# Performance work log

Hardware: AMD Instinct MI355X
Metric: run time of the kernel (lower is better)

## Reference

```python
import jax, jax.numpy as jnp
import numpy as np

D_IN = 16
D_OUT = 8
HIDDEN = 64


def setup_inputs() -> dict:
    key = jax.random.key(0)
    ks = jax.random.split(key, 8)
    B = 524288
    x = jax.random.normal(ks[0], (B, D_IN), dtype=jnp.float32)
    # scalar attention weights for the two attention blocks, shape [2, 1]
    wq = jax.random.normal(ks[1], (2, 1), dtype=jnp.float32)
    wk = jax.random.normal(ks[2], (2, 1), dtype=jnp.float32)
    wv = jax.random.normal(ks[3], (2, 1), dtype=jnp.float32)
    # hidden: Linear(16 -> HIDDEN), output: Linear(HIDDEN -> 8)
    lim_h = 1.0 / np.sqrt(D_IN)
    Wh = jax.random.uniform(ks[4], (HIDDEN, D_IN), minval=-lim_h, maxval=lim_h, dtype=jnp.float32)
    bh = jax.random.uniform(ks[5], (HIDDEN,), minval=-lim_h, maxval=lim_h, dtype=jnp.float32)
    lim_o = 1.0 / np.sqrt(HIDDEN)
    Wo = jax.random.uniform(ks[6], (D_OUT, HIDDEN), minval=-lim_o, maxval=lim_o, dtype=jnp.float32)
    bo = jax.random.uniform(ks[7], (D_OUT,), minval=-lim_o, maxval=lim_o, dtype=jnp.float32)
    return {"x": x, "wq": wq, "wk": wk, "wv": wv, "Wh": Wh, "bh": bh, "Wo": Wo, "bo": bo}


def _self_attention(x, q, k, v):
    # x: [B, D]; q, k, v: scalars. Q=K=V are scalar-scaled copies of x.
    Q = q * x  # [B, D]
    K = k * x
    V = v * x
    # Alpha[b, i, j] = K[b, i] * Q[b, j]  (outer product, matches Kt @ Q)
    Alpha = K[:, :, None] * Q[:, None, :]  # [B, D, D]
    A = jax.nn.softmax(Alpha, axis=2)
    # O[b, j] = sum_i V[b, i] * A[b, i, j]  (matches V @ AlphaD)
    return jnp.einsum('bi,bij->bj', V, A)  # [B, D]


def reference(x, wq, wk, wv, Wh, bh, Wo, bo):
    o1 = _self_attention(x[:, 0:16], wq[0, 0], wk[0, 0], wv[0, 0])  # [B, 16]
    x1 = jax.nn.sigmoid(o1 @ Wh.T + bh)                              # [B, HIDDEN]
    x2 = x1 @ Wo.T + bo                                              # [B, 8]
    o2 = _self_attention(x2, wq[1, 0], wk[1, 0], wv[1, 0])          # [B, 8]
    w = jax.nn.softmax(o2, axis=1)                                   # [B, 8]
    # out = x[:, None, 8:16] @ w[:, :, None]  -> [B, 1, 1]
    out = jnp.einsum('bi,bi->b', x[:, 8:16], w)[:, None, None]
    return out
```

## Files before the change

kernel.cpp:

```cpp
#include <hip/hip_runtime.h>


typedef float v2f __attribute__((ext_vector_type(2)));

#define LOG2E 1.44269504088896340736f
#define ROWS 4

__device__ __forceinline__ float rcpf(float a) { return __builtin_amdgcn_rcpf(a); }

#if __has_builtin(__builtin_amdgcn_exp2f)
__device__ __forceinline__ float exp2_fast(float a) { return __builtin_amdgcn_exp2f(a); }
#else
__device__ __forceinline__ float exp2_fast(float a) { return __expf(0.6931471805599453f * a); }
#endif

__global__ __launch_bounds__(256, 2) void fused_attn_mlp(
    const float* __restrict__ x,
    const float* __restrict__ wq,
    const float* __restrict__ wk,
    const float* __restrict__ wv,
    const float* __restrict__ Wh,
    const float* __restrict__ bh,
    const float* __restrict__ Wo,
    const float* __restrict__ bo,
    float* __restrict__ out,
    int B)
{
    const int t = threadIdx.x;
    const int b0 = blockIdx.x * (256 * ROWS) + t;

    bool valid[ROWS];
    #pragma unroll
    for (int r = 0; r < ROWS; ++r) valid[r] = (b0 + r * 256) < B;

    float4 xraw[ROWS][4];
    #pragma unroll
    for (int r = 0; r < ROWS; ++r) {
        if (valid[r]) {
            const float4* xr = reinterpret_cast<const float4*>(x) + (size_t)(b0 + r * 256) * 4;
            xraw[r][0] = xr[0]; xraw[r][1] = xr[1]; xraw[r][2] = xr[2]; xraw[r][3] = xr[3];
        } else {
            xraw[r][0] = xraw[r][1] = xraw[r][2] = xraw[r][3] = float4{0.f,0.f,0.f,0.f};
        }
    }

    __shared__ float sWh[64 * 16];
    __shared__ float sWoT[64 * 8];
    __shared__ float sbh[64];
    {
        const float4* src = reinterpret_cast<const float4*>(Wh);
        float4* dst = reinterpret_cast<float4*>(sWh);
        dst[t] = src[t];
    }
    #pragma unroll
    for (int r = t; r < 512; r += 256) {
        const int h = r >> 3, o = r & 7;
        sWoT[h * 8 + o] = Wo[o * 64 + h];
    }
    if (t < 64) sbh[t] = bh[t];
    __syncthreads();

    float xs[ROWS][16];
    v2f xv2[ROWS][8];
    #pragma unroll
    for (int r = 0; r < ROWS; ++r) {
        xs[r][0]=xraw[r][0].x; xs[r][1]=xraw[r][0].y; xs[r][2]=xraw[r][0].z; xs[r][3]=xraw[r][0].w;
        xs[r][4]=xraw[r][1].x; xs[r][5]=xraw[r][1].y; xs[r][6]=xraw[r][1].z; xs[r][7]=xraw[r][1].w;
        xs[r][8]=xraw[r][2].x; xs[r][9]=xraw[r][2].y; xs[r][10]=xraw[r][2].z; xs[r][11]=xraw[r][2].w;
        xs[r][12]=xraw[r][3].x; xs[r][13]=xraw[r][3].y; xs[r][14]=xraw[r][3].z; xs[r][15]=xraw[r][3].w;
        #pragma unroll
        for (int p = 0; p < 8; ++p) { v2f v; v[0]=xs[r][2*p]; v[1]=xs[r][2*p+1]; xv2[r][p]=v; }
    }

    const float kq1 = wk[0] * wq[0] * LOG2E;
    const float v1  = wv[0];

    float xmx[ROWS], xmn[ROWS];
    #pragma unroll
    for (int r = 0; r < ROWS; ++r) {
        float mx = xs[r][0], mn = xs[r][0];
        #pragma unroll
        for (int i = 1; i < 16; ++i) { mx = fmaxf(mx, xs[r][i]); mn = fminf(mn, xs[r][i]); }
        xmx[r] = mx; xmn[r] = mn;
    }

    v2f o1v[ROWS][8];
    #pragma unroll
    for (int r = 0; r < ROWS; ++r)
        #pragma unroll
        for (int p = 0; p < 8; ++p) o1v[r][p] = (v2f)(0.f);

    #pragma unroll
    for (int i = 0; i < 16; ++i) {
        v2f e2[ROWS][8];
        float w[ROWS];
        #pragma unroll
        for (int r = 0; r < ROWS; ++r) {
            const float c = kq1 * xs[r][i];
            const float m = fmaxf(c * xmx[r], c * xmn[r]);
            v2f cc; cc[0]=c; cc[1]=c;
            v2f mm; mm[0]=m; mm[1]=m;
            #pragma unroll
            for (int p = 0; p < 8; ++p) {
                v2f a = cc * xv2[r][p] - mm;
                v2f e; e[0] = exp2_fast(a[0]); e[1] = exp2_fast(a[1]);
                e2[r][p] = e;
            }
            v2f s01 = e2[r][0] + e2[r][1];
            v2f s23 = e2[r][2] + e2[r][3];
            v2f s45 = e2[r][4] + e2[r][5];
            v2f s67 = e2[r][6] + e2[r][7];
            v2f sv  = (s01 + s23) + (s45 + s67);
            w[r] = v1 * xs[r][i] * rcpf(sv[0] + sv[1]);
        }
        #pragma unroll
        for (int r = 0; r < ROWS; ++r) {
            v2f ww; ww[0]=w[r]; ww[1]=w[r];
            #pragma unroll
            for (int p = 0; p < 8; ++p) o1v[r][p] += ww * e2[r][p];
        }
    }

    v2f x2v[ROWS][4];
    #pragma unroll
    for (int r = 0; r < ROWS; ++r)
        #pragma unroll
        for (int p = 0; p < 4; ++p) { v2f v; v[0]=bo[2*p]; v[1]=bo[2*p+1]; x2v[r][p]=v; }

    #pragma unroll 2
    for (int g = 0; g < 16; ++g) {
        float apre[ROWS][4];
        #pragma unroll
        for (int hh = 0; hh < 4; ++hh) {
            const int h = g * 4 + hh;
            const v2f* wh = reinterpret_cast<const v2f*>(sWh + h * 16);
            v2f whr[8];
            #pragma unroll
            for (int p = 0; p < 8; ++p) whr[p] = wh[p];
            #pragma unroll
            for (int r = 0; r < ROWS; ++r) {
                v2f acc = whr[0] * o1v[r][0];
                #pragma unroll
                for (int p = 1; p < 8; ++p) acc += whr[p] * o1v[r][p];
                apre[r][hh] = acc[0] + acc[1] + sbh[h];
            }
        }
        float sg[ROWS][4];
        #pragma unroll
        for (int r = 0; r < ROWS; ++r) {
            float d[4];
            #pragma unroll
            for (int hh = 0; hh < 4; ++hh) {
                const float la = fminf(-apre[r][hh] * LOG2E, 30.f);
                d[hh] = 1.f + exp2_fast(la);
            }
            const float p01  = d[0] * d[1];
            const float p012 = p01 * d[2];
            const float rq   = rcpf(p012 * d[3]);
            const float i3 = rq * p012;
            const float tq = rq * d[3];
            const float i2 = tq * p01;
            const float t2 = tq * d[2];
            sg[r][0] = t2 * d[1];
            sg[r][1] = t2 * d[0];
            sg[r][2] = i2;
            sg[r][3] = i3;
        }
        #pragma unroll
        for (int hh = 0; hh < 4; ++hh) {
            const int h = g * 4 + hh;
            const v2f* wo = reinterpret_cast<const v2f*>(sWoT + h * 8);
            v2f wor[4];
            #pragma unroll
            for (int p = 0; p < 4; ++p) wor[p] = wo[p];
            #pragma unroll
            for (int r = 0; r < ROWS; ++r) {
                v2f sgv; sgv[0]=sg[r][hh]; sgv[1]=sg[r][hh];
                #pragma unroll
                for (int p = 0; p < 4; ++p) x2v[r][p] += wor[p] * sgv;
            }
        }
    }

    const float kq2 = wk[1] * wq[1] * LOG2E;
    const float v2s = wv[1] * LOG2E;

    float ys[ROWS][8];
    float ymx[ROWS], ymn[ROWS];
    #pragma unroll
    for (int r = 0; r < ROWS; ++r) {
        #pragma unroll
        for (int i = 0; i < 8; ++i) ys[r][i] = x2v[r][i >> 1][i & 1];
        float mx = ys[r][0], mn = ys[r][0];
        #pragma unroll
        for (int i = 1; i < 8; ++i) { mx = fmaxf(mx, ys[r][i]); mn = fminf(mn, ys[r][i]); }
        ymx[r] = mx; ymn[r] = mn;
    }

    v2f o2v[ROWS][4];
    #pragma unroll
    for (int r = 0; r < ROWS; ++r)
        #pragma unroll
        for (int p = 0; p < 4; ++p) o2v[r][p] = (v2f)(0.f);

    #pragma unroll
    for (int i = 0; i < 8; ++i) {
        v2f e2[ROWS][4];
        float w[ROWS];
        #pragma unroll
        for (int r = 0; r < ROWS; ++r) {
            const float c = kq2 * ys[r][i];
            const float m = fmaxf(c * ymx[r], c * ymn[r]);
            v2f cc; cc[0]=c; cc[1]=c;
            v2f mm; mm[0]=m; mm[1]=m;
            #pragma unroll
            for (int p = 0; p < 4; ++p) {
                v2f a = cc * x2v[r][p] - mm;
                v2f e; e[0] = exp2_fast(a[0]); e[1] = exp2_fast(a[1]);
                e2[r][p] = e;
            }
            v2f sv = (e2[r][0] + e2[r][1]) + (e2[r][2] + e2[r][3]);
            w[r] = v2s * ys[r][i] * rcpf(sv[0] + sv[1]);
        }
        #pragma unroll
        for (int r = 0; r < ROWS; ++r) {
            v2f ww; ww[0]=w[r]; ww[1]=w[r];
            #pragma unroll
            for (int p = 0; p < 4; ++p) o2v[r][p] += ww * e2[r][p];
        }
    }

    #pragma unroll
    for (int r = 0; r < ROWS; ++r) {
        float o2s[8];
        #pragma unroll
        for (int i = 0; i < 8; ++i) o2s[i] = o2v[r][i >> 1][i & 1];
        float m2 = o2s[0];
        #pragma unroll
        for (int i = 1; i < 8; ++i) m2 = fmaxf(m2, o2s[i]);
        v2f mm2; mm2[0]=m2; mm2[1]=m2;
        v2f se = (v2f)(0.f), de = (v2f)(0.f);
        #pragma unroll
        for (int p = 0; p < 4; ++p) {
            v2f a = o2v[r][p] - mm2;
            v2f e; e[0] = exp2_fast(a[0]); e[1] = exp2_fast(a[1]);
            se += e;
            v2f xp; xp[0]=xs[r][8+2*p]; xp[1]=xs[r][9+2*p];
            de += xp * e;
        }
        if (valid[r]) out[b0 + r * 256] = (de[0] + de[1]) * rcpf(se[0] + se[1]);
    }
}

extern "C" void kernel_launch(void* const* d_in, const int* in_sizes, int n_in,
                              void* d_out, int out_size, void* d_ws, size_t ws_size,
                              hipStream_t stream) {
    const float* x  = (const float*)d_in[0];
    const float* wq = (const float*)d_in[1];
    const float* wk = (const float*)d_in[2];
    const float* wv = (const float*)d_in[3];
    const float* Wh = (const float*)d_in[4];
    const float* bh = (const float*)d_in[5];
    const float* Wo = (const float*)d_in[6];
    const float* bo = (const float*)d_in[7];
    float* out = (float*)d_out;

    const int B = in_sizes[0] / 16;
    const int block = 256;
    const int rows_per_block = block * ROWS;
    const int grid = (B + rows_per_block - 1) / rows_per_block;
    fused_attn_mlp<<<grid, block, 0, stream>>>(x, wq, wk, wv, Wh, bh, Wo, bo, out, B);
}
```

Baseline: 129.4 us.

## Read MLP weights directly from global memory, drop LDS staging, halve rows per thread

Removes the shared-memory staging of Wh, Wo and bh along with the block barrier. Weights are now loaded straight from global memory, where every thread reads the same uniform addresses, which the compiler can turn into scalar loads. Rows per thread drop from 4 to 2 and launch bounds ask for 4 blocks per CU, trading weight reuse per load for higher occupancy. The risk is more load instructions per row and strided 4-byte reads of the transposed Wo.

Result: no change. 127.0 us (-1.9%).

```diff
diff --git a/kernel.cpp b/kernel.cpp
--- a/kernel.cpp
+++ b/kernel.cpp
@@ -4,7 +4,7 @@
 typedef float v2f __attribute__((ext_vector_type(2)));
 
 #define LOG2E 1.44269504088896340736f
-#define ROWS 4
+#define ROWS 2
 
 __device__ __forceinline__ float rcpf(float a) { return __builtin_amdgcn_rcpf(a); }
 
@@ -14,7 +14,7 @@
 __device__ __forceinline__ float exp2_fast(float a) { return __expf(0.6931471805599453f * a); }
 #endif
 
-__global__ __launch_bounds__(256, 2) void fused_attn_mlp(
+__global__ __launch_bounds__(256, 4) void fused_attn_mlp(
     const float* __restrict__ x,
     const float* __restrict__ wq,
     const float* __restrict__ wk,
@@ -44,22 +44,6 @@
         }
     }
 
-    __shared__ float sWh[64 * 16];
-    __shared__ float sWoT[64 * 8];
-    __shared__ float sbh[64];
-    {
-        const float4* src = reinterpret_cast<const float4*>(Wh);
-        float4* dst = reinterpret_cast<float4*>(sWh);
-        dst[t] = src[t];
-    }
-    #pragma unroll
-    for (int r = t; r < 512; r += 256) {
-        const int h = r >> 3, o = r & 7;
-        sWoT[h * 8 + o] = Wo[o * 64 + h];
-    }
-    if (t < 64) sbh[t] = bh[t];
-    __syncthreads();
-
     float xs[ROWS][16];
     v2f xv2[ROWS][8];
     #pragma unroll
@@ -127,22 +111,25 @@
         #pragma unroll
         for (int p = 0; p < 4; ++p) { v2f v; v[0]=bo[2*p]; v[1]=bo[2*p+1]; x2v[r][p]=v; }
 
+    const v2f* Wh2 = reinterpret_cast<const v2f*>(Wh);
+    const v2f* Wo2 = reinterpret_cast<const v2f*>(Wo);
+
     #pragma unroll 2
     for (int g = 0; g < 16; ++g) {
         float apre[ROWS][4];
         #pragma unroll
         for (int hh = 0; hh < 4; ++hh) {
             const int h = g * 4 + hh;
-            const v2f* wh = reinterpret_cast<const v2f*>(sWh + h * 16);
             v2f whr[8];
             #pragma unroll
-            for (int p = 0; p < 8; ++p) whr[p] = wh[p];
+            for (int p = 0; p < 8; ++p) whr[p] = Wh2[h * 8 + p];
+            const float bhh = bh[h];
             #pragma unroll
             for (int r = 0; r < ROWS; ++r) {
                 v2f acc = whr[0] * o1v[r][0];
                 #pragma unroll
                 for (int p = 1; p < 8; ++p) acc += whr[p] * o1v[r][p];
-                apre[r][hh] = acc[0] + acc[1] + sbh[h];
+                apre[r][hh] = acc[0] + acc[1] + bhh;
             }
         }
         float sg[ROWS][4];
@@ -169,15 +156,16 @@
         #pragma unroll
         for (int hh = 0; hh < 4; ++hh) {
             const int h = g * 4 + hh;
-            const v2f* wo = reinterpret_cast<const v2f*>(sWoT + h * 8);
-            v2f wor[4];
-            #pragma unroll
-            for (int p = 0; p < 4; ++p) wor[p] = wo[p];
-            #pragma unroll
-            for (int r = 0; r < ROWS; ++r) {
-                v2f sgv; sgv[0]=sg[r][hh]; sgv[1]=sg[r][hh];
+            #pragma unroll
+            for (int p = 0; p < 4; ++p) {
+                v2f wo2;
+                wo2[0] = Wo[(2 * p) * 64 + h];
+                wo2[1] = Wo[(2 * p + 1) * 64 + h];
                 #pragma unroll
-                for (int p = 0; p < 4; ++p) x2v[r][p] += wor[p] * sgv;
+                for (int r = 0; r < ROWS; ++r) {
+                    v2f sgv; sgv[0] = sg[r][hh]; sgv[1] = sg[r][hh];
+                    x2v[r][p] += wo2 * sgv;
+                }
             }
         }
     }
```
